# Kernel optimization log

Hardware: AMD Instinct MI355X
Metric: run time of the kernel (lower is better)

## Reference

```python
import jax, jax.numpy as jnp
import numpy as np

D = 128
NP, NA, NI = 200_000, 150_000, 10_000
E_PP, E_PA, E_AP, E_AI, E_IA = 600_000, 500_000, 500_000, 150_000, 150_000
EPS = 1e-5


def _edges(key, n_src, n_dst, n_edges):
    k1, k2 = jax.random.split(key)
    src = jax.random.randint(k1, (n_edges,), 0, n_src, dtype=jnp.int32)
    dst = jax.random.randint(k2, (n_edges,), 0, n_dst, dtype=jnp.int32)
    return jnp.stack([src, dst])  # [2, E]


def setup_inputs() -> dict:
    key = jax.random.key(0)
    ks = jax.random.split(key, 12)
    x_paper = jax.random.normal(ks[0], (NP, D), dtype=jnp.float32)
    x_author = jax.random.normal(ks[1], (NA, D), dtype=jnp.float32)
    x_inst = jax.random.normal(ks[2], (NI, D), dtype=jnp.float32)
    e_pp = _edges(ks[3], NP, NP, E_PP)
    e_pa = _edges(ks[4], NP, NA, E_PA)
    e_ap = _edges(ks[5], NA, NP, E_AP)
    e_ai = _edges(ks[6], NA, NI, E_AI)
    e_ia = _edges(ks[7], NI, NA, E_IA)
    scale = 1.0 / np.sqrt(D)
    Wl = jax.random.normal(ks[8], (11, D, D), dtype=jnp.float32) * scale
    Wr = jax.random.normal(ks[9], (11, D, D), dtype=jnp.float32) * scale
    bL = jnp.zeros((11, D), dtype=jnp.float32)
    bn_g = jnp.ones((5, D), dtype=jnp.float32)
    bn_b = jnp.zeros((5, D), dtype=jnp.float32)
    return dict(x_paper=x_paper, x_author=x_author, x_inst=x_inst,
                e_pp=e_pp, e_pa=e_pa, e_ap=e_ap, e_ai=e_ai, e_ia=e_ia,
                Wl=Wl, bL=bL, Wr=Wr, bn_g=bn_g, bn_b=bn_b)


def _sage(x_src, x_dst, edge, n_dst, wl, b, wr):
    # SAGEConv: lin_l(mean of neighbor feats) + lin_r(x_dst); root skipped if x_dst is None
    src, dst = edge[0], edge[1]
    msg = x_src[src]                                   # [E, D] gather
    agg = jax.ops.segment_sum(msg, dst, num_segments=n_dst)
    cnt = jax.ops.segment_sum(jnp.ones((edge.shape[1], 1), msg.dtype), dst, num_segments=n_dst)
    mean = agg / jnp.maximum(cnt, 1.0)
    out = mean @ wl + b
    if x_dst is not None:
        out = out + x_dst @ wr
    return out


def _bn(x, g, b):
    # BatchNorm1d, training-mode (biased batch stats)
    m = x.mean(0)
    v = jnp.mean((x - m) ** 2, 0)
    return (x - m) * jax.lax.rsqrt(v + EPS) * g + b


def _hetero_sage(x_paper, x_author, x_inst, e_pp, e_pa, e_ap, e_ai, e_ia,
                 Wl, bL, Wr, bn_g, bn_b):
    n_p, n_a, n_i = x_paper.shape[0], x_author.shape[0], x_inst.shape[0]
    # Layer 0: only edge types with src == 'paper'
    p = _sage(x_paper, x_paper, e_pp, n_p, Wl[0], bL[0], Wr[0])
    a = _sage(x_paper, x_author, e_pa, n_a, Wl[1], bL[1], Wr[1])
    p = _bn(jax.nn.relu(p), bn_g[0], bn_b[0])
    a = _bn(jax.nn.relu(a), bn_g[1], bn_b[1])
    # Layer 1: edge types with src != 'institution' (institution feats absent -> no root for ai)
    p1 = (_sage(p, p, e_pp, n_p, Wl[2], bL[2], Wr[2])
          + _sage(a, p, e_ap, n_p, Wl[4], bL[4], Wr[4]))
    a1 = _sage(p, a, e_pa, n_a, Wl[3], bL[3], Wr[3])
    i1 = _sage(a, None, e_ai, n_i, Wl[5], bL[5], Wr[5])
    p1 = _bn(jax.nn.relu(p1), bn_g[2], bn_b[2])
    a1 = _bn(jax.nn.relu(a1), bn_g[3], bn_b[3])
    i1 = _bn(jax.nn.relu(i1), bn_g[4], bn_b[4])
    # Layer 2 (output layer): all edge types, no relu/BN
    p2 = (_sage(p1, p1, e_pp, n_p, Wl[6], bL[6], Wr[6])
          + _sage(a1, p1, e_ap, n_p, Wl[8], bL[8], Wr[8]))
    a2 = (_sage(p1, a1, e_pa, n_a, Wl[7], bL[7], Wr[7])
          + _sage(i1, a1, e_ia, n_a, Wl[10], bL[10], Wr[10]))
    i2 = _sage(a1, i1, e_ai, n_i, Wl[9], bL[9], Wr[9])
    return p2, a2, i2


def reference(x_paper, x_author, x_inst, e_pp, e_pa, e_ap, e_ai, e_ia,
              Wl, bL, Wr, bn_g, bn_b):
    return _hetero_sage(x_paper, x_author, x_inst, e_pp, e_pa, e_ap, e_ai, e_ia,
                        Wl, bL, Wr, bn_g, bn_b)
```

## Files before the change

### kernel.cpp

```cpp
#include <hip/hip_runtime.h>

typedef unsigned short u16;
typedef unsigned int u32;
typedef unsigned long long u64;
typedef __attribute__((ext_vector_type(4))) float f32x4;
typedef __attribute__((ext_vector_type(8))) short s16x8;

__device__ __forceinline__ float bf2f(u16 u) {
  union { u32 i; float f; } x;
  x.i = ((u32)u) << 16;
  return x.f;
}
__device__ __forceinline__ u16 f2bf(float f) {
  union { float f; u32 i; } u;
  u.f = f;
  u32 r = u.i + 0x7fffu + ((u.i >> 16) & 1u);
  return (u16)(r >> 16);
}

static inline int nblkA(long long n) { return (int)((n + 255) / 256); }

__global__ void HeteroGraphSAGE_52931176955955_kernel(float* p, long long n) {
  long long i = (long long)blockIdx.x * 256 + threadIdx.x;
  if (i < n) p[i] = 0.0f;
}

__global__ void g_wprep(const float* Wl, const float* Wr, u16* wt, int total) {
  int idx = blockIdx.x * 256 + threadIdx.x;
  if (idx >= total) return;
  int w = idx >> 14;
  int r = idx & 16383;
  int n = r >> 7, k = r & 127;
  float v;
  if (w < 11) v = Wl[w * 16384 + k * 128 + n];
  else if (w < 22) v = Wr[(w - 11) * 16384 + k * 128 + n];
  else {
    int a = (w == 22) ? 2 : (w == 23) ? 6 : 7;
    int b = (w == 22) ? 4 : (w == 23) ? 8 : 10;
    v = Wr[a * 16384 + k * 128 + n] + Wr[b * 16384 + k * 128 + n];
  }
  wt[idx] = f2bf(v);
}

__global__ void g_bprep(const float* bL, float* cb) {
  int c = threadIdx.x;
  cb[c]       = bL[2 * 128 + c] + bL[4 * 128 + c];
  cb[128 + c] = bL[6 * 128 + c] + bL[8 * 128 + c];
  cb[256 + c] = bL[7 * 128 + c] + bL[10 * 128 + c];
}

__global__ void g_cvt(const float* x, u16* o, long long n4) {
  long long i = (long long)blockIdx.x * 256 + threadIdx.x;
  if (i >= n4) return;
  f32x4 v = *(const f32x4*)(x + (i << 2));
  u64 p = ((u64)f2bf(v.x)) | (((u64)f2bf(v.y)) << 16) |
          (((u64)f2bf(v.z)) << 32) | (((u64)f2bf(v.w)) << 48);
  *(u64*)(o + (i << 2)) = p;
}

__global__ void g_deg(const int* e, int E, int* deg) {
  int w = blockIdx.x * 256 + threadIdx.x;
  if (w >= E) return;
  atomicAdd(deg + e[E + w], 1);
}

__global__ void g_bsum(const int* deg, int n, int C, int* bsum) {
  __shared__ int ws[4];
  int b = blockIdx.x, tid = threadIdx.x;
  int lane = tid & 63, wv = tid >> 6;
  int lo = b * C, hi = lo + C; if (hi > n) hi = n;
  int s = 0;
  for (int i = lo + tid; i < hi; i += 256) s += deg[i];
  for (int o = 32; o > 0; o >>= 1) s += __shfl_down(s, o);
  if (lane == 0) ws[wv] = s;
  __syncthreads();
  if (tid == 0) bsum[b] = ws[0] + ws[1] + ws[2] + ws[3];
}

__global__ void g_scan_write(const int* deg, int n, int C, const int* bsum,
                             int* rp, int* cur) {
  __shared__ int ws[4];
  __shared__ int bc;
  int b = blockIdx.x, tid = threadIdx.x;
  int lane = tid & 63, wv = tid >> 6;

  int v = bsum[tid];
  int s = (tid < b) ? v : 0;
  for (int o = 32; o > 0; o >>= 1) s += __shfl_down(s, o);
  if (lane == 0) ws[wv] = s;
  __syncthreads();
  if (tid == 0) bc = ws[0] + ws[1] + ws[2] + ws[3];
  __syncthreads();
  int base = bc;

  if (b == 0) {
    __syncthreads();
    int t = v;
    for (int o = 32; o > 0; o >>= 1) t += __shfl_down(t, o);
    if (lane == 0) ws[wv] = t;
    __syncthreads();
    if (tid == 0) rp[n] = ws[0] + ws[1] + ws[2] + ws[3];
  }

  int lo = b * C, hi = lo + C; if (hi > n) hi = n;
  for (int t0 = lo; t0 < hi; t0 += 256) {
    int i = t0 + tid;
    int d = (i < hi) ? deg[i] : 0;
    int x = d;
    for (int o = 1; o < 64; o <<= 1) {
      int t = __shfl_up(x, o);
      if (lane >= o) x += t;
    }
    __syncthreads();
    if (lane == 63) ws[wv] = x;
    __syncthreads();
    int wadd = 0;
    if (wv > 0) wadd += ws[0];
    if (wv > 1) wadd += ws[1];
    if (wv > 2) wadd += ws[2];
    int excl = x + wadd - d;
    if (i < hi) {
      rp[i] = base + excl;
      cur[i] = base + excl;
    }
    base += ws[0] + ws[1] + ws[2] + ws[3];
    __syncthreads();
  }
}

__global__ void g_fill(const int* e, int E, int* cur, int* col) {
  int w = blockIdx.x * 256 + threadIdx.x;
  if (w >= E) return;
  int s = e[w];
  int d = e[E + w];
  col[atomicAdd(cur + d, 1)] = s;
}

__device__ __forceinline__ void stage_store(u16* sm, int rr, int q, const float* acc) {
  s16x8 o;
#pragma unroll
  for (int e = 0; e < 8; ++e) o[e] = (short)f2bf(acc[e]);
  int byte = (rr << 8) + (q << 4);
  int swz = byte ^ ((rr & 7) << 4);
  *(s16x8*)((char*)sm + swz) = o;
}

__global__ __launch_bounds__(256) void g_sage(
    const int* rpA, const int* colA, const u16* srcA, const float* scshA, const u16* wtlA,
    const int* rpB, const int* colB, const u16* srcB, const float* scshB, const u16* wtlB,
    const void* root, int root_f32, const float* scshR, const u16* wtr,
    const float* bias, void* out, int out_bf, int N, float* partial) {
  extern __shared__ __align__(16) char smem[];
  const int tid = threadIdx.x;
  const int r0 = blockIdx.x * 32;
  const int nbuf = 1 + (rpB ? 1 : 0) + (root ? 1 : 0);
  u16* smA = (u16*)smem;
  u16* smB = (u16*)(smem + 8192);
  u16* smR = (u16*)(smem + (size_t)(nbuf - 1) * 8192);
  float* bs = (float*)(smem + (size_t)nbuf * 8192);
  if (partial) bs[tid] = 0.f;

  for (int i = tid; i < nbuf * 512; i += 256) {
    int region = i >> 9;
    int t = i & 511;
    int rr = t >> 4, q = t & 15;
    int row = r0 + rr;
    int c0 = q * 8;
    float acc[8];
#pragma unroll
    for (int e = 0; e < 8; ++e) acc[e] = 0.f;

    bool isRoot = root && (region == nbuf - 1);
    if (isRoot) {
      if (row < N) {
        if (root_f32) {
          const float* rp_ = (const float*)root + (size_t)row * 128 + c0;
          f32x4 lo = *(const f32x4*)rp_;
          f32x4 hi = *(const f32x4*)(rp_ + 4);
          acc[0] = lo.x; acc[1] = lo.y; acc[2] = lo.z; acc[3] = lo.w;
          acc[4] = hi.x; acc[5] = hi.y; acc[6] = hi.z; acc[7] = hi.w;
        } else {
          s16x8 v = *(const s16x8*)((const u16*)root + (size_t)row * 128 + c0);
#pragma unroll
          for (int e = 0; e < 8; ++e) acc[e] = bf2f((u16)v[e]);
        }
        if (scshR) {
#pragma unroll
          for (int e = 0; e < 8; ++e)
            acc[e] = fmaxf(acc[e], 0.f) * scshR[c0 + e] + scshR[128 + c0 + e];
        }
      }
      stage_store(smR, rr, q, acc);
    } else {
      const int* rp = (region == 0) ? rpA : rpB;
      const int* col = (region == 0) ? colA : colB;
      const u16* src = (region == 0) ? srcA : srcB;
      const float* scsh = (region == 0) ? scshA : scshB;
      if (row < N) {
        int j0 = rp[row], j1 = rp[row + 1];
        if (scsh) {
          float sc[8], sh[8];
#pragma unroll
          for (int e = 0; e < 8; ++e) { sc[e] = scsh[c0 + e]; sh[e] = scsh[128 + c0 + e]; }
          for (int j = j0; j < j1; ++j) {
            s16x8 v = *(const s16x8*)(src + (size_t)col[j] * 128 + c0);
#pragma unroll
            for (int e = 0; e < 8; ++e)
              acc[e] += fmaxf(bf2f((u16)v[e]), 0.f) * sc[e] + sh[e];
          }
        } else {
          for (int j = j0; j < j1; ++j) {
            s16x8 v = *(const s16x8*)(src + (size_t)col[j] * 128 + c0);
#pragma unroll
            for (int e = 0; e < 8; ++e) acc[e] += bf2f((u16)v[e]);
          }
        }
        float inv = 1.0f / fmaxf((float)(j1 - j0), 1.0f);
#pragma unroll
        for (int e = 0; e < 8; ++e) acc[e] *= inv;
      }
      stage_store((region == 0) ? smA : smB, rr, q, acc);
    }
  }
  __syncthreads();

  const int lane = tid & 63;
  const int wv = tid >> 6;
  const int mi = lane & 15;
  const int kg = lane >> 4;
  const int m = wv >> 1;
  const int nq = (wv & 1) * 4;
  const int arow = m * 16 + mi;
  const int abase = arow << 8;
  const int amask = (arow & 7) << 4;

  f32x4 acc4[4];
#pragma unroll
  for (int t = 0; t < 4; ++t) acc4[t] = (f32x4){0.f, 0.f, 0.f, 0.f};

#pragma unroll
  for (int kt = 0; kt < 4; ++kt) {
    int k0 = kt * 32 + kg * 8;
    int off = (abase + (k0 << 1)) ^ amask;
    s16x8 afA = *(const s16x8*)((const char*)smA + off);
    s16x8 afB, afR;
    if (rpB) afB = *(const s16x8*)((const char*)smB + off);
    if (root) afR = *(const s16x8*)((const char*)smR + off);
#pragma unroll
    for (int t = 0; t < 4; ++t) {
      int cr = (nq + t) * 16 + mi;
      s16x8 b = *(const s16x8*)(wtlA + cr * 128 + k0);
      acc4[t] = __builtin_amdgcn_mfma_f32_16x16x32_bf16(afA, b, acc4[t], 0, 0, 0);
      if (rpB) {
        s16x8 b2 = *(const s16x8*)(wtlB + cr * 128 + k0);
        acc4[t] = __builtin_amdgcn_mfma_f32_16x16x32_bf16(afB, b2, acc4[t], 0, 0, 0);
      }
      if (root) {
        s16x8 b3 = *(const s16x8*)(wtr + cr * 128 + k0);
        acc4[t] = __builtin_amdgcn_mfma_f32_16x16x32_bf16(afR, b3, acc4[t], 0, 0, 0);
      }
    }
  }

  int rbase = (lane >> 4) << 2;
#pragma unroll
  for (int t = 0; t < 4; ++t) {
    int c = (nq + t) * 16 + mi;
    float bb = bias[c];
    float s = 0.f, q = 0.f;
#pragma unroll
    for (int reg = 0; reg < 4; ++reg) {
      int row = r0 + m * 16 + rbase + reg;
      if (row < N) {
        size_t o = (size_t)row * 128 + c;
        float v = acc4[t][reg] + bb;
        if (out_bf) ((u16*)out)[o] = f2bf(v);
        else        ((float*)out)[o] = v;
        if (partial) {
          float r = fmaxf(v, 0.f);
          s += r;
          q += r * r;
        }
      }
    }
    if (partial) {
      s += __shfl_xor(s, 16); s += __shfl_xor(s, 32);
      q += __shfl_xor(q, 16); q += __shfl_xor(q, 32);
      if (kg == 0) {
        atomicAdd(&bs[c], s);
        atomicAdd(&bs[128 + c], q);
      }
    }
  }
  if (partial) {
    __syncthreads();
    partial[(size_t)blockIdx.x * 256 + tid] = bs[tid];
  }
}

__global__ void g_bnred(const float* partial, int nb, float* p2) {
  int tid = threadIdx.x;
  float acc = 0.f;
  for (int blk = blockIdx.x; blk < nb; blk += 64)
    acc += partial[(size_t)blk * 256 + tid];
  p2[(size_t)blockIdx.x * 256 + tid] = acc;
}

__global__ void g_bnfin(const float* p2, const float* g, const float* b,
                        float invN, float* scsh) {
  int c = threadIdx.x;
  float s = 0.f, q = 0.f;
  for (int blk = 0; blk < 64; ++blk) {
    s += p2[(size_t)blk * 256 + c];
    q += p2[(size_t)blk * 256 + 128 + c];
  }
  float m = s * invN;
  float v = q * invN - m * m;
  float sc = rsqrtf(v + 1e-5f) * g[c];
  scsh[c] = sc;
  scsh[128 + c] = b[c] - m * sc;
}

struct Csr { int* rp; int* col; };

static void build_csr(const int* e, int E, int ndst, Csr c, int* dega, int* cur,
                      int* bsum, hipStream_t st) {
  HeteroGraphSAGE_52931176955955_kernel<<<nblkA(ndst), 256, 0, st>>>((float*)dega, ndst);
  g_deg<<<nblkA(E), 256, 0, st>>>(e, E, dega);
  int C = (ndst + 255) / 256;
  g_bsum<<<256, 256, 0, st>>>(dega, ndst, C, bsum);
  g_scan_write<<<256, 256, 0, st>>>(dega, ndst, C, bsum, c.rp, cur);
  g_fill<<<nblkA(E), 256, 0, st>>>(e, E, cur, c.col);
}

static void bn_vA(int nb, const float* g, const float* b, int n,
                  float* partial, float* p2, float* scsh, hipStream_t st) {
  g_bnred<<<64, 256, 0, st>>>(partial, nb, p2);
  g_bnfin<<<1, 128, 0, st>>>(p2, g, b, 1.0f / (float)n, scsh);
}

extern "C" void kernel_launch(void* const* d_in, const int* in_sizes, int n_in,
                              void* d_out, int out_size, void* d_ws, size_t ws_size,
                              hipStream_t stream) {
  const float* x_paper  = (const float*)d_in[0];
  const float* x_author = (const float*)d_in[1];
  const int* e_pp = (const int*)d_in[3];
  const int* e_pa = (const int*)d_in[4];
  const int* e_ap = (const int*)d_in[5];
  const int* e_ai = (const int*)d_in[6];
  const int* e_ia = (const int*)d_in[7];
  const float* Wl  = (const float*)d_in[8];
  const float* bL  = (const float*)d_in[9];
  const float* Wr  = (const float*)d_in[10];
  const float* bng = (const float*)d_in[11];
  const float* bnb = (const float*)d_in[12];

  const int NP = in_sizes[0] / 128;
  const int NA = in_sizes[1] / 128;
  const int NI = in_sizes[2] / 128;
  const int Epp = in_sizes[3] / 2;
  const int Epa = in_sizes[4] / 2;
  const int Eap = in_sizes[5] / 2;
  const int Eai = in_sizes[6] / 2;
  const int Eia = in_sizes[7] / 2;

  const int nbP = (NP + 31) / 32;
  const int nbA = (NA + 31) / 32;
  const int nbI = (NI + 31) / 32;

  char* ws = (char*)d_ws;
  size_t off = 0;
  u16* xp   = (u16*)(ws + off);   off += (size_t)NP * 256;
  u16* h_p1 = (u16*)(ws + off);   off += (size_t)NP * 256;
  u16* h_a1 = (u16*)(ws + off);   off += (size_t)NA * 256;
  u16* wt   = (u16*)(ws + off);   off += (size_t)25 * 16384 * 2;
  Csr cpp; cpp.rp = (int*)(ws + off); off += (size_t)(NP + 1) * 4;
  Csr cpa; cpa.rp = (int*)(ws + off); off += (size_t)(NA + 1) * 4;
  Csr cap; cap.rp = (int*)(ws + off); off += (size_t)(NP + 1) * 4;
  Csr cai; cai.rp = (int*)(ws + off); off += (size_t)(NI + 1) * 4;
  Csr cia; cia.rp = (int*)(ws + off); off += (size_t)(NA + 1) * 4;
  cpp.col = (int*)(ws + off); off += (size_t)Epp * 4;
  cpa.col = (int*)(ws + off); off += (size_t)Epa * 4;
  cap.col = (int*)(ws + off); off += (size_t)Eap * 4;
  cai.col = (int*)(ws + off); off += (size_t)Eai * 4;
  cia.col = (int*)(ws + off); off += (size_t)Eia * 4;
  int* dega = (int*)(ws + off);      off += (size_t)NP * 4;
  int* cur  = (int*)(ws + off);      off += (size_t)NP * 4;
  int* bsum = (int*)(ws + off);      off += 1024;
  float* partial = (float*)(ws + off); off += (size_t)nbP * 1024;
  float* p2    = (float*)(ws + off); off += 64 * 1024;
  float* scsh0 = (float*)(ws + off); off += 1024;
  float* scsh1 = (float*)(ws + off); off += 1024;
  float* scsh2 = (float*)(ws + off); off += 1024;
  float* scsh3 = (float*)(ws + off); off += 1024;
  float* scsh4 = (float*)(ws + off); off += 1024;
  float* cb    = (float*)(ws + off); off += 3 * 512;

  float* outp = (float*)d_out;
  float* outa = outp + (size_t)NP * 128;
  float* outi = outa + (size_t)NA * 128;
  u16* h_p0 = (u16*)outp;
  u16* h_a0 = (u16*)outa;
  u16* h_i1 = (u16*)outp + (size_t)NP * 128;

  g_wprep<<<nblkA(25 * 16384), 256, 0, stream>>>(Wl, Wr, wt, 25 * 16384);
  g_bprep<<<1, 128, 0, stream>>>(bL, cb);
  g_cvt<<<nblkA((long long)NP * 32), 256, 0, stream>>>(x_paper, xp, (long long)NP * 32);
  build_csr(e_pp, Epp, NP, cpp, dega, cur, bsum, stream);
  build_csr(e_pa, Epa, NA, cpa, dega, cur, bsum, stream);
  build_csr(e_ap, Eap, NP, cap, dega, cur, bsum, stream);
  build_csr(e_ai, Eai, NI, cai, dega, cur, bsum, stream);
  build_csr(e_ia, Eia, NA, cia, dega, cur, bsum, stream);

  const float* nof = (const float*)0;
  const int* noi = (const int*)0;
  const u16* nou = (const u16*)0;
  float* nop = (float*)0;

#define WT(i) (wt + (size_t)(i) * 16384)

  g_sage<<<nbP, 256, 2 * 8192 + 1024, stream>>>(
      cpp.rp, cpp.col, xp, nof, WT(0), noi, noi, nou, nof, nou,
      xp, 0, nof, WT(11), bL + 0 * 128, h_p0, 1, NP, partial);
  bn_vA(nbP, bng + 0 * 128, bnb + 0 * 128, NP, partial, p2, scsh0, stream);
  g_sage<<<nbA, 256, 2 * 8192 + 1024, stream>>>(
      cpa.rp, cpa.col, xp, nof, WT(1), noi, noi, nou, nof, nou,
      x_author, 1, nof, WT(12), bL + 1 * 128, h_a0, 1, NA, partial);
  bn_vA(nbA, bng + 1 * 128, bnb + 1 * 128, NA, partial, p2, scsh1, stream);

  g_sage<<<nbP, 256, 3 * 8192 + 1024, stream>>>(
      cpp.rp, cpp.col, h_p0, scsh0, WT(2), cap.rp, cap.col, h_a0, scsh1, WT(4),
      h_p0, 0, scsh0, WT(22), cb, h_p1, 1, NP, partial);
  bn_vA(nbP, bng + 2 * 128, bnb + 2 * 128, NP, partial, p2, scsh2, stream);
  g_sage<<<nbA, 256, 2 * 8192 + 1024, stream>>>(
      cpa.rp, cpa.col, h_p0, scsh0, WT(3), noi, noi, nou, nof, nou,
      h_a0, 0, scsh1, WT(14), bL + 3 * 128, h_a1, 1, NA, partial);
  bn_vA(nbA, bng + 3 * 128, bnb + 3 * 128, NA, partial, p2, scsh3, stream);
  g_sage<<<nbI, 256, 1 * 8192 + 1024, stream>>>(
      cai.rp, cai.col, h_a0, scsh1, WT(5), noi, noi, nou, nof, nou,
      (const void*)0, 0, nof, nou, bL + 5 * 128, h_i1, 1, NI, partial);
  bn_vA(nbI, bng + 4 * 128, bnb + 4 * 128, NI, partial, p2, scsh4, stream);

  g_sage<<<nbA, 256, 3 * 8192, stream>>>(
      cpa.rp, cpa.col, h_p1, scsh2, WT(7), cia.rp, cia.col, h_i1, scsh4, WT(10),
      h_a1, 0, scsh3, WT(24), cb + 256, outa, 0, NA, nop);
  g_sage<<<nbI, 256, 2 * 8192, stream>>>(
      cai.rp, cai.col, h_a1, scsh3, WT(9), noi, noi, nou, nof, nou,
      h_i1, 0, scsh4, WT(20), bL + 9 * 128, outi, 0, NI, nop);
  g_sage<<<nbP, 256, 3 * 8192, stream>>>(
      cpp.rp, cpp.col, h_p1, scsh2, WT(6), cap.rp, cap.col, h_a1, scsh3, WT(8),
      h_p1, 0, scsh2, WT(23), cb + 128, outp, 0, NP, nop);

#undef WT
  (void)n_in; (void)ws_size; (void)out_size;
}
```

Before: 1.527 ms.

## Gather neighbor rows with one wavefront per row and prefetch next neighbor

The gather/mean stage of the SAGE kernel now assigns each destination row to a whole 64-lane wavefront, with each lane loading 2 bf16 values (4 bytes). Previously a 16-lane group handled a row with 16-byte loads per lane. The change also software-pipelines the neighbor loop so the next row's load is issued before the current one is accumulated, and it hoists the scale/shift loads out of the row loop. The aim is more independent rows in flight and better latency hiding on the irregular gathers. The trade-off is narrower per-lane loads, more loop iterations per thread, and serialized rows per wave; some helpers were also renamed.

```diff
diff --git a/kernel.cpp b/kernel.cpp
--- a/kernel.cpp
+++ b/kernel.cpp
@@ -18,7 +18,7 @@
   return (u16)(r >> 16);
 }
 
-static inline int nblkA(long long n) { return (int)((n + 255) / 256); }
+static inline int nblkC(long long n) { return (int)((n + 255) / 256); }
 
 __global__ void HeteroGraphSAGE_52931176955955_kernel(float* p, long long n) {
   long long i = (long long)blockIdx.x * 256 + threadIdx.x;
@@ -134,15 +134,6 @@
   int s = e[w];
   int d = e[E + w];
   col[atomicAdd(cur + d, 1)] = s;
-}
-
-__device__ __forceinline__ void stage_store(u16* sm, int rr, int q, const float* acc) {
-  s16x8 o;
-#pragma unroll
-  for (int e = 0; e < 8; ++e) o[e] = (short)f2bf(acc[e]);
-  int byte = (rr << 8) + (q << 4);
-  int swz = byte ^ ((rr & 7) << 4);
-  *(s16x8*)((char*)sm + swz) = o;
 }
 
 __global__ __launch_bounds__(256) void g_sage(
@@ -160,71 +151,69 @@
   float* bs = (float*)(smem + (size_t)nbuf * 8192);
   if (partial) bs[tid] = 0.f;
 
-  for (int i = tid; i < nbuf * 512; i += 256) {
-    int region = i >> 9;
-    int t = i & 511;
-    int rr = t >> 4, q = t & 15;
-    int row = r0 + rr;
-    int c0 = q * 8;
-    float acc[8];
-#pragma unroll
-    for (int e = 0; e < 8; ++e) acc[e] = 0.f;
-
+  const int lane = tid & 63;
+  const int wvv = tid >> 6;
+
+  for (int region = 0; region < nbuf; ++region) {
     bool isRoot = root && (region == nbuf - 1);
-    if (isRoot) {
+    const int* rp   = (region == 0) ? rpA : rpB;
+    const int* col  = (region == 0) ? colA : colB;
+    const u16* src  = (region == 0) ? srcA : srcB;
+    const float* scsh = isRoot ? scshR : ((region == 0) ? scshA : scshB);
+    u16* sm = isRoot ? smR : ((region == 0) ? smA : smB);
+    float sc0 = 1.f, sc1 = 1.f, sh0 = 0.f, sh1 = 0.f;
+    const bool hasT = (scsh != 0);
+    if (hasT) {
+      sc0 = scsh[2 * lane];       sc1 = scsh[2 * lane + 1];
+      sh0 = scsh[128 + 2 * lane]; sh1 = scsh[128 + 2 * lane + 1];
+    }
+    for (int rr = wvv; rr < 32; rr += 4) {
+      int row = r0 + rr;
+      float a0 = 0.f, a1 = 0.f;
       if (row < N) {
-        if (root_f32) {
-          const float* rp_ = (const float*)root + (size_t)row * 128 + c0;
-          f32x4 lo = *(const f32x4*)rp_;
-          f32x4 hi = *(const f32x4*)(rp_ + 4);
-          acc[0] = lo.x; acc[1] = lo.y; acc[2] = lo.z; acc[3] = lo.w;
-          acc[4] = hi.x; acc[5] = hi.y; acc[6] = hi.z; acc[7] = hi.w;
+        if (isRoot) {
+          if (root_f32) {
+            const float* q = (const float*)root + (size_t)row * 128 + 2 * lane;
+            a0 = q[0]; a1 = q[1];
+          } else {
+            u32 v = *(const u32*)((const u16*)root + (size_t)row * 128 + 2 * lane);
+            a0 = bf2f((u16)v); a1 = bf2f((u16)(v >> 16));
+          }
+          if (hasT) {
+            a0 = fmaxf(a0, 0.f) * sc0 + sh0;
+            a1 = fmaxf(a1, 0.f) * sc1 + sh1;
+          }
         } else {
-          s16x8 v = *(const s16x8*)((const u16*)root + (size_t)row * 128 + c0);
-#pragma unroll
-          for (int e = 0; e < 8; ++e) acc[e] = bf2f((u16)v[e]);
-        }
-        if (scshR) {
-#pragma unroll
-          for (int e = 0; e < 8; ++e)
-            acc[e] = fmaxf(acc[e], 0.f) * scshR[c0 + e] + scshR[128 + c0 + e];
+          int j0 = rp[row], j1 = rp[row + 1];
+          if (j0 < j1) {
+            u32 vc = *(const u32*)(src + (size_t)col[j0] * 128 + 2 * lane);
+            for (int j = j0 + 1; j < j1; ++j) {
+              u32 vn = *(const u32*)(src + (size_t)col[j] * 128 + 2 * lane);
+              float f0 = bf2f((u16)vc), f1 = bf2f((u16)(vc >> 16));
+              if (hasT) {
+                a0 += fmaxf(f0, 0.f) * sc0 + sh0;
+                a1 += fmaxf(f1, 0.f) * sc1 + sh1;
+              } else { a0 += f0; a1 += f1; }
+              vc = vn;
+            }
+            float f0 = bf2f((u16)vc), f1 = bf2f((u16)(vc >> 16));
+            if (hasT) {
+              a0 += fmaxf(f0, 0.f) * sc0 + sh0;
+              a1 += fmaxf(f1, 0.f) * sc1 + sh1;
+            } else { a0 += f0; a1 += f1; }
+            float inv = 1.0f / (float)(j1 - j0);
+            a0 *= inv; a1 *= inv;
+          }
         }
       }
-      stage_store(smR, rr, q, acc);
-    } else {
-      const int* rp = (region == 0) ? rpA : rpB;
-      const int* col = (region == 0) ? colA : colB;
-      const u16* src = (region == 0) ? srcA : srcB;
-      const float* scsh = (region == 0) ? scshA : scshB;
-      if (row < N) {
-        int j0 = rp[row], j1 = rp[row + 1];
-        if (scsh) {
-          float sc[8], sh[8];
-#pragma unroll
-          for (int e = 0; e < 8; ++e) { sc[e] = scsh[c0 + e]; sh[e] = scsh[128 + c0 + e]; }
-          for (int j = j0; j < j1; ++j) {
-            s16x8 v = *(const s16x8*)(src + (size_t)col[j] * 128 + c0);
-#pragma unroll
-            for (int e = 0; e < 8; ++e)
-              acc[e] += fmaxf(bf2f((u16)v[e]), 0.f) * sc[e] + sh[e];
-          }
-        } else {
-          for (int j = j0; j < j1; ++j) {
-            s16x8 v = *(const s16x8*)(src + (size_t)col[j] * 128 + c0);
-#pragma unroll
-            for (int e = 0; e < 8; ++e) acc[e] += bf2f((u16)v[e]);
-          }
-        }
-        float inv = 1.0f / fmaxf((float)(j1 - j0), 1.0f);
-#pragma unroll
-        for (int e = 0; e < 8; ++e) acc[e] *= inv;
-      }
-      stage_store((region == 0) ? smA : smB, rr, q, acc);
+      u32 o = ((u32)f2bf(a0)) | (((u32)f2bf(a1)) << 16);
+      int byte = (rr << 8) + (lane << 2);
+      int swz = byte ^ ((rr & 7) << 4);
+      *(u32*)((char*)sm + swz) = o;
     }
   }
   __syncthreads();
 
-  const int lane = tid & 63;
   const int wv = tid >> 6;
   const int mi = lane & 15;
   const int kg = lane >> 4;
@@ -325,15 +314,15 @@
 
 static void build_csr(const int* e, int E, int ndst, Csr c, int* dega, int* cur,
                       int* bsum, hipStream_t st) {
-  HeteroGraphSAGE_52931176955955_kernel<<<nblkA(ndst), 256, 0, st>>>((float*)dega, ndst);
-  g_deg<<<nblkA(E), 256, 0, st>>>(e, E, dega);
+  HeteroGraphSAGE_52931176955955_kernel<<<nblkC(ndst), 256, 0, st>>>((float*)dega, ndst);
+  g_deg<<<nblkC(E), 256, 0, st>>>(e, E, dega);
   int C = (ndst + 255) / 256;
   g_bsum<<<256, 256, 0, st>>>(dega, ndst, C, bsum);
   g_scan_write<<<256, 256, 0, st>>>(dega, ndst, C, bsum, c.rp, cur);
-  g_fill<<<nblkA(E), 256, 0, st>>>(e, E, cur, c.col);
-}
-
-static void bn_vA(int nb, const float* g, const float* b, int n,
+  g_fill<<<nblkC(E), 256, 0, st>>>(e, E, cur, c.col);
+}
+
+static void bn_vC(int nb, const float* g, const float* b, int n,
                   float* partial, float* p2, float* scsh, hipStream_t st) {
   g_bnred<<<64, 256, 0, st>>>(partial, nb, p2);
   g_bnfin<<<1, 128, 0, st>>>(p2, g, b, 1.0f / (float)n, scsh);
@@ -403,9 +392,9 @@
   u16* h_a0 = (u16*)outa;
   u16* h_i1 = (u16*)outp + (size_t)NP * 128;
 
-  g_wprep<<<nblkA(25 * 16384), 256, 0, stream>>>(Wl, Wr, wt, 25 * 16384);
+  g_wprep<<<nblkC(25 * 16384), 256, 0, stream>>>(Wl, Wr, wt, 25 * 16384);
   g_bprep<<<1, 128, 0, stream>>>(bL, cb);
-  g_cvt<<<nblkA((long long)NP * 32), 256, 0, stream>>>(x_paper, xp, (long long)NP * 32);
+  g_cvt<<<nblkC((long long)NP * 32), 256, 0, stream>>>(x_paper, xp, (long long)NP * 32);
   build_csr(e_pp, Epp, NP, cpp, dega, cur, bsum, stream);
   build_csr(e_pa, Epa, NA, cpa, dega, cur, bsum, stream);
   build_csr(e_ap, Eap, NP, cap, dega, cur, bsum, stream);
@@ -422,24 +411,24 @@
   g_sage<<<nbP, 256, 2 * 8192 + 1024, stream>>>(
       cpp.rp, cpp.col, xp, nof, WT(0), noi, noi, nou, nof, nou,
       xp, 0, nof, WT(11), bL + 0 * 128, h_p0, 1, NP, partial);
-  bn_vA(nbP, bng + 0 * 128, bnb + 0 * 128, NP, partial, p2, scsh0, stream);
+  bn_vC(nbP, bng + 0 * 128, bnb + 0 * 128, NP, partial, p2, scsh0, stream);
   g_sage<<<nbA, 256, 2 * 8192 + 1024, stream>>>(
       cpa.rp, cpa.col, xp, nof, WT(1), noi, noi, nou, nof, nou,
       x_author, 1, nof, WT(12), bL + 1 * 128, h_a0, 1, NA, partial);
-  bn_vA(nbA, bng + 1 * 128, bnb + 1 * 128, NA, partial, p2, scsh1, stream);
+  bn_vC(nbA, bng + 1 * 128, bnb + 1 * 128, NA, partial, p2, scsh1, stream);
 
   g_sage<<<nbP, 256, 3 * 8192 + 1024, stream>>>(
       cpp.rp, cpp.col, h_p0, scsh0, WT(2), cap.rp, cap.col, h_a0, scsh1, WT(4),
       h_p0, 0, scsh0, WT(22), cb, h_p1, 1, NP, partial);
-  bn_vA(nbP, bng + 2 * 128, bnb + 2 * 128, NP, partial, p2, scsh2, stream);
+  bn_vC(nbP, bng + 2 * 128, bnb + 2 * 128, NP, partial, p2, scsh2, stream);
   g_sage<<<nbA, 256, 2 * 8192 + 1024, stream>>>(
       cpa.rp, cpa.col, h_p0, scsh0, WT(3), noi, noi, nou, nof, nou,
       h_a0, 0, scsh1, WT(14), bL + 3 * 128, h_a1, 1, NA, partial);
-  bn_vA(nbA, bng + 3 * 128, bnb + 3 * 128, NA, partial, p2, scsh3, stream);
+  bn_vC(nbA, bng + 3 * 128, bnb + 3 * 128, NA, partial, p2, scsh3, stream);
   g_sage<<<nbI, 256, 1 * 8192 + 1024, stream>>>(
       cai.rp, cai.col, h_a0, scsh1, WT(5), noi, noi, nou, nof, nou,
       (const void*)0, 0, nof, nou, bL + 5 * 128, h_i1, 1, NI, partial);
-  bn_vA(nbI, bng + 4 * 128, bnb + 4 * 128, NI, partial, p2, scsh4, stream);
+  bn_vC(nbI, bng + 4 * 128, bnb + 4 * 128, NI, partial, p2, scsh4, stream);
 
   g_sage<<<nbA, 256, 3 * 8192, stream>>>(
       cpa.rp, cpa.col, h_p1, scsh2, WT(7), cia.rp, cia.col, h_i1, scsh4, WT(10),
```

New measurement: 1.788 ms. 1.17x slower.

## Parallelize neighbor aggregation over edges with LDS float atomics per tile

Applied to the files above, without the earlier changes.

The per-row sequential neighbor gather loop is replaced by an edge-parallel scheme. Each block loads its 32-row CSR offsets into LDS, spreads the tile's edges over all threads, finds each edge's row by binary search, and accumulates into an fp32 LDS tile with atomicAdd. A second pass divides by degree, applies the BN affine, and writes the swizzled bf16 staging. This targets load imbalance and low memory-level parallelism from uneven degrees, at the cost of larger LDS use (lower occupancy), LDS atomic contention and extra barriers.

```diff
diff --git a/kernel.cpp b/kernel.cpp
--- a/kernel.cpp
+++ b/kernel.cpp
@@ -18,7 +18,7 @@
   return (u16)(r >> 16);
 }
 
-static inline int nblkA(long long n) { return (int)((n + 255) / 256); }
+static inline int nblkD(long long n) { return (int)((n + 255) / 256); }
 
 __global__ void HeteroGraphSAGE_52931176955955_kernel(float* p, long long n) {
   long long i = (long long)blockIdx.x * 256 + threadIdx.x;
@@ -153,76 +153,118 @@
   extern __shared__ __align__(16) char smem[];
   const int tid = threadIdx.x;
   const int r0 = blockIdx.x * 32;
-  const int nbuf = 1 + (rpB ? 1 : 0) + (root ? 1 : 0);
+  const int nA = 1 + (rpB ? 1 : 0);
+  float* tileF0 = (float*)smem;
+  float* tileF1 = (float*)(smem + 16384);
   u16* smA = (u16*)smem;
-  u16* smB = (u16*)(smem + 8192);
-  u16* smR = (u16*)(smem + (size_t)(nbuf - 1) * 8192);
-  float* bs = (float*)(smem + (size_t)nbuf * 8192);
+  u16* smB = (u16*)(smem + 16384);
+  u16* smR = (u16*)(smem + (size_t)nA * 16384);
+  int* rps0 = (int*)(smem + (size_t)nA * 16384 + (root ? 8192 : 0));
+  int* rps1 = rps0 + 64;
+  float* bs = (float*)((char*)rps0 + 512);
   if (partial) bs[tid] = 0.f;
 
-  for (int i = tid; i < nbuf * 512; i += 256) {
-    int region = i >> 9;
-    int t = i & 511;
-    int rr = t >> 4, q = t & 15;
-    int row = r0 + rr;
-    int c0 = q * 8;
-    float acc[8];
-#pragma unroll
-    for (int e = 0; e < 8; ++e) acc[e] = 0.f;
-
-    bool isRoot = root && (region == nbuf - 1);
-    if (isRoot) {
+  if (tid < 33) {
+    int r = r0 + tid; if (r > N) r = N;
+    rps0[tid] = rpA[r];
+  }
+  if (rpB && tid >= 64 && tid < 97) {
+    int r = r0 + (tid - 64); if (r > N) r = N;
+    rps1[tid - 64] = rpB[r];
+  }
+  for (int i = tid; i < nA * 4096; i += 256) ((float*)smem)[i] = 0.f;
+  __syncthreads();
+
+  for (int region = 0; region < nA; ++region) {
+    const int* rps = region ? rps1 : rps0;
+    const int* col = region ? colB : colA;
+    const u16* src = region ? srcB : srcA;
+    const bool hasT = (region ? scshB : scshA) != 0;
+    float* tf = region ? tileF1 : tileF0;
+    int jlo = rps[0];
+    int ne = rps[32] - jlo;
+    for (int t = tid; t < ne * 16; t += 256) {
+      int j = t >> 4, q = t & 15;
+      int jj = jlo + j;
+      int s = col[jj];
+      s16x8 v = *(const s16x8*)(src + (size_t)s * 128 + q * 8);
+      int lo = 0, hi = 32;
+#pragma unroll
+      for (int it = 0; it < 5; ++it) {
+        int mid = (lo + hi) >> 1;
+        if (rps[mid] <= jj) lo = mid; else hi = mid;
+      }
+      float* dst = tf + lo * 128 + q * 8;
+#pragma unroll
+      for (int e = 0; e < 8; ++e) {
+        float f = bf2f((u16)v[e]);
+        if (hasT) f = fmaxf(f, 0.f);
+        atomicAdd(dst + e, f);
+      }
+    }
+  }
+  if (root) {
+    for (int i = tid; i < 512; i += 256) {
+      int rr = i >> 4, q = i & 15;
+      int row = r0 + rr;
+      int c0 = q * 8;
+      float a[8];
+#pragma unroll
+      for (int e = 0; e < 8; ++e) a[e] = 0.f;
       if (row < N) {
         if (root_f32) {
           const float* rp_ = (const float*)root + (size_t)row * 128 + c0;
           f32x4 lo = *(const f32x4*)rp_;
           f32x4 hi = *(const f32x4*)(rp_ + 4);
-          acc[0] = lo.x; acc[1] = lo.y; acc[2] = lo.z; acc[3] = lo.w;
-          acc[4] = hi.x; acc[5] = hi.y; acc[6] = hi.z; acc[7] = hi.w;
+          a[0] = lo.x; a[1] = lo.y; a[2] = lo.z; a[3] = lo.w;
+          a[4] = hi.x; a[5] = hi.y; a[6] = hi.z; a[7] = hi.w;
         } else {
           s16x8 v = *(const s16x8*)((const u16*)root + (size_t)row * 128 + c0);
 #pragma unroll
-          for (int e = 0; e < 8; ++e) acc[e] = bf2f((u16)v[e]);
+          for (int e = 0; e < 8; ++e) a[e] = bf2f((u16)v[e]);
         }
         if (scshR) {
 #pragma unroll
           for (int e = 0; e < 8; ++e)
-            acc[e] = fmaxf(acc[e], 0.f) * scshR[c0 + e] + scshR[128 + c0 + e];
+            a[e] = fmaxf(a[e], 0.f) * scshR[c0 + e] + scshR[128 + c0 + e];
         }
       }
-      stage_store(smR, rr, q, acc);
-    } else {
-      const int* rp = (region == 0) ? rpA : rpB;
-      const int* col = (region == 0) ? colA : colB;
-      const u16* src = (region == 0) ? srcA : srcB;
-      const float* scsh = (region == 0) ? scshA : scshB;
-      if (row < N) {
-        int j0 = rp[row], j1 = rp[row + 1];
-        if (scsh) {
-          float sc[8], sh[8];
-#pragma unroll
-          for (int e = 0; e < 8; ++e) { sc[e] = scsh[c0 + e]; sh[e] = scsh[128 + c0 + e]; }
-          for (int j = j0; j < j1; ++j) {
-            s16x8 v = *(const s16x8*)(src + (size_t)col[j] * 128 + c0);
-#pragma unroll
-            for (int e = 0; e < 8; ++e)
-              acc[e] += fmaxf(bf2f((u16)v[e]), 0.f) * sc[e] + sh[e];
-          }
-        } else {
-          for (int j = j0; j < j1; ++j) {
-            s16x8 v = *(const s16x8*)(src + (size_t)col[j] * 128 + c0);
-#pragma unroll
-            for (int e = 0; e < 8; ++e) acc[e] += bf2f((u16)v[e]);
-          }
-        }
-        float inv = 1.0f / fmaxf((float)(j1 - j0), 1.0f);
-#pragma unroll
-        for (int e = 0; e < 8; ++e) acc[e] *= inv;
-      }
-      stage_store((region == 0) ? smA : smB, rr, q, acc);
+      stage_store(smR, rr, q, a);
     }
   }
   __syncthreads();
+
+  {
+    const int rr = tid >> 3;
+    const int c0 = (tid & 7) * 16;
+    for (int region = 0; region < nA; ++region) {
+      const float* scsh = region ? scshB : scshA;
+      const int* rps = region ? rps1 : rps0;
+      const float* tf = region ? tileF1 : tileF0;
+      u16* sm = region ? smB : smA;
+      int deg = rps[rr + 1] - rps[rr];
+      float inv = (deg > 0) ? 1.0f / (float)deg : 0.0f;
+      float vr[16];
+#pragma unroll
+      for (int e = 0; e < 16; ++e) vr[e] = tf[rr * 128 + c0 + e] * inv;
+      if (scsh && deg > 0) {
+#pragma unroll
+        for (int e = 0; e < 16; ++e)
+          vr[e] = vr[e] * scsh[c0 + e] + scsh[128 + c0 + e];
+      }
+      __syncthreads();
+#pragma unroll
+      for (int h = 0; h < 2; ++h) {
+        s16x8 o;
+#pragma unroll
+        for (int e = 0; e < 8; ++e) o[e] = (short)f2bf(vr[h * 8 + e]);
+        int byte = (rr << 8) + ((c0 + h * 8) << 1);
+        int swz = byte ^ ((rr & 7) << 4);
+        *(s16x8*)((char*)sm + swz) = o;
+      }
+      __syncthreads();
+    }
+  }
 
   const int lane = tid & 63;
   const int wv = tid >> 6;
@@ -325,18 +367,22 @@
 
 static void build_csr(const int* e, int E, int ndst, Csr c, int* dega, int* cur,
                       int* bsum, hipStream_t st) {
-  HeteroGraphSAGE_52931176955955_kernel<<<nblkA(ndst), 256, 0, st>>>((float*)dega, ndst);
-  g_deg<<<nblkA(E), 256, 0, st>>>(e, E, dega);
+  HeteroGraphSAGE_52931176955955_kernel<<<nblkD(ndst), 256, 0, st>>>((float*)dega, ndst);
+  g_deg<<<nblkD(E), 256, 0, st>>>(e, E, dega);
   int C = (ndst + 255) / 256;
   g_bsum<<<256, 256, 0, st>>>(dega, ndst, C, bsum);
   g_scan_write<<<256, 256, 0, st>>>(dega, ndst, C, bsum, c.rp, cur);
-  g_fill<<<nblkA(E), 256, 0, st>>>(e, E, cur, c.col);
-}
-
-static void bn_vA(int nb, const float* g, const float* b, int n,
+  g_fill<<<nblkD(E), 256, 0, st>>>(e, E, cur, c.col);
+}
+
+static void bn_vD(int nb, const float* g, const float* b, int n,
                   float* partial, float* p2, float* scsh, hipStream_t st) {
   g_bnred<<<64, 256, 0, st>>>(partial, nb, p2);
   g_bnfin<<<1, 128, 0, st>>>(p2, g, b, 1.0f / (float)n, scsh);
+}
+
+static inline int lds_sz(int hasB, int hasRoot) {
+  return (1 + hasB) * 16384 + (hasRoot ? 8192 : 0) + 512 + 1024;
 }
 
 extern "C" void kernel_launch(void* const* d_in, const int* in_sizes, int n_in,
@@ -403,9 +449,9 @@
   u16* h_a0 = (u16*)outa;
   u16* h_i1 = (u16*)outp + (size_t)NP * 128;
 
-  g_wprep<<<nblkA(25 * 16384), 256, 0, stream>>>(Wl, Wr, wt, 25 * 16384);
+  g_wprep<<<nblkD(25 * 16384), 256, 0, stream>>>(Wl, Wr, wt, 25 * 16384);
   g_bprep<<<1, 128, 0, stream>>>(bL, cb);
-  g_cvt<<<nblkA((long long)NP * 32), 256, 0, stream>>>(x_paper, xp, (long long)NP * 32);
+  g_cvt<<<nblkD((long long)NP * 32), 256, 0, stream>>>(x_paper, xp, (long long)NP * 32);
   build_csr(e_pp, Epp, NP, cpp, dega, cur, bsum, stream);
   build_csr(e_pa, Epa, NA, cpa, dega, cur, bsum, stream);
   build_csr(e_ap, Eap, NP, cap, dega, cur, bsum, stream);
@@ -419,35 +465,35 @@
 
 #define WT(i) (wt + (size_t)(i) * 16384)
 
-  g_sage<<<nbP, 256, 2 * 8192 + 1024, stream>>>(
+  g_sage<<<nbP, 256, lds_sz(0, 1), stream>>>(
       cpp.rp, cpp.col, xp, nof, WT(0), noi, noi, nou, nof, nou,
       xp, 0, nof, WT(11), bL + 0 * 128, h_p0, 1, NP, partial);
-  bn_vA(nbP, bng + 0 * 128, bnb + 0 * 128, NP, partial, p2, scsh0, stream);
-  g_sage<<<nbA, 256, 2 * 8192 + 1024, stream>>>(
+  bn_vD(nbP, bng + 0 * 128, bnb + 0 * 128, NP, partial, p2, scsh0, stream);
+  g_sage<<<nbA, 256, lds_sz(0, 1), stream>>>(
       cpa.rp, cpa.col, xp, nof, WT(1), noi, noi, nou, nof, nou,
       x_author, 1, nof, WT(12), bL + 1 * 128, h_a0, 1, NA, partial);
-  bn_vA(nbA, bng + 1 * 128, bnb + 1 * 128, NA, partial, p2, scsh1, stream);
-
-  g_sage<<<nbP, 256, 3 * 8192 + 1024, stream>>>(
+  bn_vD(nbA, bng + 1 * 128, bnb + 1 * 128, NA, partial, p2, scsh1, stream);
+
+  g_sage<<<nbP, 256, lds_sz(1, 1), stream>>>(
       cpp.rp, cpp.col, h_p0, scsh0, WT(2), cap.rp, cap.col, h_a0, scsh1, WT(4),
       h_p0, 0, scsh0, WT(22), cb, h_p1, 1, NP, partial);
-  bn_vA(nbP, bng + 2 * 128, bnb + 2 * 128, NP, partial, p2, scsh2, stream);
-  g_sage<<<nbA, 256, 2 * 8192 + 1024, stream>>>(
+  bn_vD(nbP, bng + 2 * 128, bnb + 2 * 128, NP, partial, p2, scsh2, stream);
+  g_sage<<<nbA, 256, lds_sz(0, 1), stream>>>(
       cpa.rp, cpa.col, h_p0, scsh0, WT(3), noi, noi, nou, nof, nou,
       h_a0, 0, scsh1, WT(14), bL + 3 * 128, h_a1, 1, NA, partial);
-  bn_vA(nbA, bng + 3 * 128, bnb + 3 * 128, NA, partial, p2, scsh3, stream);
-  g_sage<<<nbI, 256, 1 * 8192 + 1024, stream>>>(
+  bn_vD(nbA, bng + 3 * 128, bnb + 3 * 128, NA, partial, p2, scsh3, stream);
+  g_sage<<<nbI, 256, lds_sz(0, 0), stream>>>(
       cai.rp, cai.col, h_a0, scsh1, WT(5), noi, noi, nou, nof, nou,
       (const void*)0, 0, nof, nou, bL + 5 * 128, h_i1, 1, NI, partial);
-  bn_vA(nbI, bng + 4 * 128, bnb + 4 * 128, NI, partial, p2, scsh4, stream);
-
-  g_sage<<<nbA, 256, 3 * 8192, stream>>>(
+  bn_vD(nbI, bng + 4 * 128, bnb + 4 * 128, NI, partial, p2, scsh4, stream);
+
+  g_sage<<<nbA, 256, lds_sz(1, 1), stream>>>(
       cpa.rp, cpa.col, h_p1, scsh2, WT(7), cia.rp, cia.col, h_i1, scsh4, WT(10),
       h_a1, 0, scsh3, WT(24), cb + 256, outa, 0, NA, nop);
-  g_sage<<<nbI, 256, 2 * 8192, stream>>>(
+  g_sage<<<nbI, 256, lds_sz(0, 1), stream>>>(
       cai.rp, cai.col, h_a1, scsh3, WT(9), noi, noi, nou, nof, nou,
       h_i1, 0, scsh4, WT(20), bL + 9 * 128, outi, 0, NI, nop);
-  g_sage<<<nbP, 256, 3 * 8192, stream>>>(
+  g_sage<<<nbP, 256, lds_sz(1, 1), stream>>>(
       cpp.rp, cpp.col, h_p1, scsh2, WT(6), cap.rp, cap.col, h_a1, scsh3, WT(8),
       h_p1, 0, scsh2, WT(23), cb + 128, outp, 0, NP, nop);
 
```

New measurement: 4.011 ms (median of 2 runs). +162.8%, slower.
